# Kernel tuning notes

Hardware: AMD Instinct MI355X
Metric: run time of the kernel (lower is better)

Reference implementation:

```python
import jax, jax.numpy as jnp
import numpy as np

TAU = 2.0        # LIFNode default tau
V_TH = 1.0       # v_threshold
BN_EPS = 1e-5


def setup_inputs() -> dict:
    key = jax.random.key(0)
    k1, k2 = jax.random.split(key)
    T, B, C, V, E = 16, 512, 2, 25, 256
    x = jax.random.normal(k1, (T, B, C, V), dtype=jnp.float32)
    W = jax.random.normal(k2, (E, C), dtype=jnp.float32) * 0.5  # conv1x1 weight [out,in]
    gamma = jnp.ones((E,), dtype=jnp.float32)
    beta = jnp.zeros((E,), dtype=jnp.float32)
    return {"x": x, "W": W, "gamma": gamma, "beta": beta}


def reference(x, W, gamma, beta):
    # x: [T, B, C, V]; conv1d(k=1) == channel-mixing matmul
    y = jnp.einsum('tbcv,ec->tbev', x, W)  # [T, B, E, V]
    # BatchNorm1d in training mode: stats over (T*B, V) per channel
    mean = jnp.mean(y, axis=(0, 1, 3), keepdims=True)
    var = jnp.var(y, axis=(0, 1, 3), keepdims=True)
    y = (y - mean) * jax.lax.rsqrt(var + BN_EPS)
    y = y * gamma[None, None, :, None] + beta[None, None, :, None]
    # Multi-step LIF: v += (x - (v - v_reset))/tau; spike = v >= v_th; hard reset to v_reset=0
    v0 = jnp.zeros(y.shape[1:], dtype=y.dtype)  # [B, E, V]
    def step(v, xt):
        v = v + (xt - v) / TAU
        spike = (v >= V_TH).astype(v.dtype)
        v = v * (1.0 - spike)  # hard reset, v_reset = 0
        return v, spike
    _, spikes = jax.lax.scan(step, v0, y)
    return spikes  # [T, B, E, V]
```

## Files before the change

### kernel.cpp

```cpp
#include <hip/hip_runtime.h>
#include <math.h>

constexpr int T = 16, B = 512, C = 2, V = 25, E = 256;
constexpr int EV  = E * V;
constexpr int BEV = B * EV;
constexpr int XT  = B * C * V;
constexpr int NB  = 1600;
constexpr int CHUNKS = 25;
constexpr int BPC = 64;
constexpr float NF = 204800.0f;

typedef float f32x4 __attribute__((ext_vector_type(4)));

#define WS_M32(ws) ((float*)(ws))
#define WS_R32(ws) ((float*)(ws) + E)

template<int PASS>
__global__ void __launch_bounds__(64) k_bs(const float* __restrict__ x,
                                           const float* __restrict__ W,
                                           const float* __restrict__ ws,
                                           float* __restrict__ bs) {
    __shared__ __align__(16) float sm0[128];
    __shared__ __align__(16) float sm1[128];
    int p  = blockIdx.x;
    int q0 = p * 128;
    {
        int tid = threadIdx.x;
        int qA = q0 + tid;           int rA = qA / 25;
        int qB = q0 + tid + 64;      int rB = qB / 25;
        sm0[tid]      = x[25 * rA + qA];
        sm0[tid + 64] = x[25 * rB + qB];
        sm1[tid]      = x[25 * rA + qA + 25];
        sm1[tid + 64] = x[25 * rB + qB + 25];
    }
    __syncthreads();

    float w0[4], w1[4], mn[4];
    #pragma unroll
    for (int u = 0; u < 4; u++) {
        int e = threadIdx.x + 64 * u;
        w0[u] = W[e * 2 + 0];
        w1[u] = W[e * 2 + 1];
        mn[u] = (PASS == 1) ? WS_M32(ws)[e] : 0.0f;
    }

    float r[4][8];
    #pragma unroll
    for (int m = 0; m < 32; m++) {
        f32x4 a4 = *reinterpret_cast<const f32x4*>(&sm0[4 * m]);
        f32x4 b4 = *reinterpret_cast<const f32x4*>(&sm1[4 * m]);
        #pragma unroll
        for (int j2 = 0; j2 < 4; j2++) {
            int k = 4 * m + j2;
            int j = k & 7;
            #pragma unroll
            for (int u = 0; u < 4; u++) {
                float y = __fadd_rn(__fmul_rn(w0[u], a4[j2]),
                                    __fmul_rn(w1[u], b4[j2]));
                if (PASS == 1) {
                    float d = __fsub_rn(y, mn[u]);
                    y = __fmul_rn(d, d);
                }
                r[u][j] = (k < 8) ? y : __fadd_rn(r[u][j], y);
            }
        }
    }
    #pragma unroll
    for (int u = 0; u < 4; u++) {
        bs[p * 256 + threadIdx.x + 64 * u] =
            __fadd_rn(__fadd_rn(__fadd_rn(r[u][0], r[u][1]),
                                __fadd_rn(r[u][2], r[u][3])),
                      __fadd_rn(__fadd_rn(r[u][4], r[u][5]),
                                __fadd_rn(r[u][6], r[u][7])));
    }
}

template<int WHICH>
__global__ void __launch_bounds__(256) k_comb(const float* __restrict__ bs,
                                              float* __restrict__ ws) {
    __shared__ float cb[NB];
    __shared__ float csum[CHUNKS];
    int e = blockIdx.x;
    for (int i = threadIdx.x; i < NB; i += 256) cb[i] = bs[i * 256 + e];
    __syncthreads();
    if (threadIdx.x < CHUNKS) {
        int c = threadIdx.x;
        float t[BPC];
        #pragma unroll
        for (int i = 0; i < BPC; i++) t[i] = cb[c * BPC + i];
        #pragma unroll
        for (int m = BPC / 2; m >= 1; m >>= 1) {
            #pragma unroll
            for (int i = 0; i < m; i++)
                t[i] = __fadd_rn(t[2 * i], t[2 * i + 1]);
        }
        csum[c] = t[0];
    }
    __syncthreads();
    if (threadIdx.x == 0) {
        float acc = 0.0f;
        #pragma unroll
        for (int c = 0; c < CHUNKS; c++) acc = __fadd_rn(acc, csum[c]);
        if (WHICH == 0) {
            WS_M32(ws)[e] = __fdiv_rn(acc, NF);
        } else {
            float var = __fdiv_rn(acc, NF);
            WS_R32(ws)[e] = __fdiv_rn(1.0f, __fsqrt_rn(__fadd_rn(var, 1e-5f)));
        }
    }
}

__global__ void __launch_bounds__(256) k_main(const float* __restrict__ x,
                                              const float* __restrict__ W,
                                              const float* __restrict__ g,
                                              const float* __restrict__ bta,
                                              const float* __restrict__ ws,
                                              float* __restrict__ out) {
    __shared__ float sx[2 * T * 50];
    int blk = blockIdx.x;
    int gi0 = blk * 1024;
    int b0  = gi0 / EV;
    int nb  = ((gi0 + 1023) / EV == b0) ? 1 : 2;
    for (int i = threadIdx.x; i < nb * 800; i += 256) {
        int bi  = i / 800;
        int r   = i - bi * 800;
        int tt  = r / 50;
        sx[i] = x[(b0 + bi) * 50 + tt * XT + (r - tt * 50)];
    }
    __syncthreads();

    int gi  = gi0 + threadIdx.x * 4;
    int b   = gi / EV;
    int rem = gi - b * EV;
    int e0  = rem / V;
    int v0  = rem - e0 * V;
    int sb  = (b - b0) * 800;
    int e1  = (e0 < E - 1) ? e0 + 1 : e0;
    float w00 = W[e0 * 2], w01 = W[e0 * 2 + 1];
    float w10 = W[e1 * 2], w11 = W[e1 * 2 + 1];
    float mn0 = WS_M32(ws)[e0], mn1 = WS_M32(ws)[e1];
    float rs0 = WS_R32(ws)[e0], rs1 = WS_R32(ws)[e1];
    float ga0 = g[e0],  ga1 = g[e1];
    float be0 = bta[e0], be1 = bta[e1];

    float wA[4], wB[4], mn[4], rs[4], ga[4], be[4];
    int   vv[4];
    #pragma unroll
    for (int j = 0; j < 4; j++) {
        int  vj = v0 + j;
        bool cr = (vj >= V);
        vv[j] = cr ? vj - V : vj;
        wA[j] = cr ? w10 : w00;  wB[j] = cr ? w11 : w01;
        mn[j] = cr ? mn1 : mn0;  rs[j] = cr ? rs1 : rs0;
        ga[j] = cr ? ga1 : ga0;  be[j] = cr ? be1 : be0;
    }

    float vm[4] = {0.0f, 0.0f, 0.0f, 0.0f};
    #pragma unroll
    for (int t = 0; t < T; t++) {
        f32x4 o;
        #pragma unroll
        for (int j = 0; j < 4; j++) {
            float x0 = sx[sb + t * 50 + vv[j]];
            float x1 = sx[sb + t * 50 + 25 + vv[j]];
            float y = __fadd_rn(__fmul_rn(wA[j], x0), __fmul_rn(wB[j], x1));
            y = __fmul_rn(__fsub_rn(y, mn[j]), rs[j]);
            y = __fadd_rn(__fmul_rn(y, ga[j]), be[j]);
            float d = __fmul_rn(__fsub_rn(y, vm[j]), 0.5f);
            vm[j] = __fadd_rn(vm[j], d);
            bool sp = (vm[j] >= 1.0f);
            o[j] = sp ? 1.0f : 0.0f;
            if (sp) vm[j] = 0.0f;
        }
        *reinterpret_cast<f32x4*>(&out[(size_t)t * BEV + gi]) = o;
    }
}

extern "C" void kernel_launch(void* const* d_in, const int* in_sizes, int n_in,
                              void* d_out, int out_size, void* d_ws, size_t ws_size,
                              hipStream_t stream) {
    (void)in_sizes; (void)n_in; (void)out_size; (void)ws_size;
    const float* x  = (const float*)d_in[0];
    const float* W  = (const float*)d_in[1];
    const float* g  = (const float*)d_in[2];
    const float* bb = (const float*)d_in[3];
    float* ws = (float*)d_ws;
    float* bs = (float*)d_out;

    k_bs<0><<<NB, 64, 0, stream>>>(x, W, ws, bs);
    k_comb<0><<<E, 256, 0, stream>>>(bs, ws);
    k_bs<1><<<NB, 64, 0, stream>>>(x, W, ws, bs);
    k_comb<1><<<E, 256, 0, stream>>>(bs, ws);
    k_main<<<BEV / 1024, 256, 0, stream>>>(x, W, g, bb, ws, (float*)d_out);
}
```

Before: 233.5 us.

## Restructure main LIF kernel to per-channel thread mapping without shared-memory staging

The main kernel now maps each thread to one (e, v) pair, with 32 lanes per channel of which 25 are active. Each block loops over 8 tiles of 8 channels for one batch. The shared-memory staging of x is dropped in favour of direct global loads, which are broadcast across channels and should hit cache. The per-thread 4-element vector and its wrap-around select logic are gone, but stores become scalar with 7 of every 32 lanes idle, so store efficiency and vectorization drop. The grid shrinks to 2048 blocks, each iterating serially over its tiles.

```diff
diff --git a/kernel.cpp b/kernel.cpp
--- a/kernel.cpp
+++ b/kernel.cpp
@@ -110,69 +110,50 @@
     }
 }
 
+constexpr int MAIN_TILES  = 16384;
+constexpr int TILES_PER_B = 8;
+constexpr int MAIN_GRID   = MAIN_TILES / TILES_PER_B;
+
 __global__ void __launch_bounds__(256) k_main(const float* __restrict__ x,
                                               const float* __restrict__ W,
                                               const float* __restrict__ g,
                                               const float* __restrict__ bta,
                                               const float* __restrict__ ws,
                                               float* __restrict__ out) {
-    __shared__ float sx[2 * T * 50];
-    int blk = blockIdx.x;
-    int gi0 = blk * 1024;
-    int b0  = gi0 / EV;
-    int nb  = ((gi0 + 1023) / EV == b0) ? 1 : 2;
-    for (int i = threadIdx.x; i < nb * 800; i += 256) {
-        int bi  = i / 800;
-        int r   = i - bi * 800;
-        int tt  = r / 50;
-        sx[i] = x[(b0 + bi) * 50 + tt * XT + (r - tt * 50)];
-    }
-    __syncthreads();
+    int e_loc = threadIdx.x >> 5;
+    int v     = threadIdx.x & 31;
+    bool act  = (v < V);
+    int  vc   = act ? v : (V - 1);
 
-    int gi  = gi0 + threadIdx.x * 4;
-    int b   = gi / EV;
-    int rem = gi - b * EV;
-    int e0  = rem / V;
-    int v0  = rem - e0 * V;
-    int sb  = (b - b0) * 800;
-    int e1  = (e0 < E - 1) ? e0 + 1 : e0;
-    float w00 = W[e0 * 2], w01 = W[e0 * 2 + 1];
-    float w10 = W[e1 * 2], w11 = W[e1 * 2 + 1];
-    float mn0 = WS_M32(ws)[e0], mn1 = WS_M32(ws)[e1];
-    float rs0 = WS_R32(ws)[e0], rs1 = WS_R32(ws)[e1];
-    float ga0 = g[e0],  ga1 = g[e1];
-    float be0 = bta[e0], be1 = bta[e1];
+    #pragma unroll 1
+    for (int it = 0; it < TILES_PER_B; it++) {
+        int tl = blockIdx.x * TILES_PER_B + it;
+        int b  = tl >> 5;
+        int e  = (tl & 31) * 8 + e_loc;
+        float w0 = W[e * 2 + 0];
+        float w1 = W[e * 2 + 1];
+        float mn = WS_M32(ws)[e];
+        float rs = WS_R32(ws)[e];
+        float ga = g[e];
+        float be = bta[e];
 
-    float wA[4], wB[4], mn[4], rs[4], ga[4], be[4];
-    int   vv[4];
-    #pragma unroll
-    for (int j = 0; j < 4; j++) {
-        int  vj = v0 + j;
-        bool cr = (vj >= V);
-        vv[j] = cr ? vj - V : vj;
-        wA[j] = cr ? w10 : w00;  wB[j] = cr ? w11 : w01;
-        mn[j] = cr ? mn1 : mn0;  rs[j] = cr ? rs1 : rs0;
-        ga[j] = cr ? ga1 : ga0;  be[j] = cr ? be1 : be0;
-    }
+        const float* xb = x + b * 50 + vc;
+        size_t gbase = (size_t)b * EV + e * V + v;
 
-    float vm[4] = {0.0f, 0.0f, 0.0f, 0.0f};
-    #pragma unroll
-    for (int t = 0; t < T; t++) {
-        f32x4 o;
+        float vm = 0.0f;
         #pragma unroll
-        for (int j = 0; j < 4; j++) {
-            float x0 = sx[sb + t * 50 + vv[j]];
-            float x1 = sx[sb + t * 50 + 25 + vv[j]];
-            float y = __fadd_rn(__fmul_rn(wA[j], x0), __fmul_rn(wB[j], x1));
-            y = __fmul_rn(__fsub_rn(y, mn[j]), rs[j]);
-            y = __fadd_rn(__fmul_rn(y, ga[j]), be[j]);
-            float d = __fmul_rn(__fsub_rn(y, vm[j]), 0.5f);
-            vm[j] = __fadd_rn(vm[j], d);
-            bool sp = (vm[j] >= 1.0f);
-            o[j] = sp ? 1.0f : 0.0f;
-            if (sp) vm[j] = 0.0f;
+        for (int t = 0; t < T; t++) {
+            float x0 = xb[t * XT];
+            float x1 = xb[t * XT + 25];
+            float y = __fadd_rn(__fmul_rn(w0, x0), __fmul_rn(w1, x1));
+            y = __fmul_rn(__fsub_rn(y, mn), rs);
+            y = __fadd_rn(__fmul_rn(y, ga), be);
+            float d = __fmul_rn(__fsub_rn(y, vm), 0.5f);
+            vm = __fadd_rn(vm, d);
+            bool sp = (vm >= 1.0f);
+            if (act) out[(size_t)t * BEV + gbase] = sp ? 1.0f : 0.0f;
+            if (sp) vm = 0.0f;
         }
-        *reinterpret_cast<f32x4*>(&out[(size_t)t * BEV + gi]) = o;
     }
 }
 
@@ -191,5 +172,5 @@
     k_comb<0><<<E, 256, 0, stream>>>(bs, ws);
     k_bs<1><<<NB, 64, 0, stream>>>(x, W, ws, bs);
     k_comb<1><<<E, 256, 0, stream>>>(bs, ws);
-    k_main<<<BEV / 1024, 256, 0, stream>>>(x, W, g, bb, ws, (float*)d_out);
+    k_main<<<MAIN_GRID, 256, 0, stream>>>(x, W, g, bb, ws, (float*)d_out);
 }
```

Measured after the change: 244.8 us. 1.05x slower.
